# Kernel optimization log

Measured on AMD Instinct MI355X. Metric: run time of the kernel, lower is better.

The kernel has to match this reference:

```python
import jax, jax.numpy as jnp
import numpy as np

BASE_TEMP, MIN_TEMP, MAX_TEMP = 0.07, 0.04, 0.2
B, D = 4096, 768


def setup_inputs() -> dict:
    key = jax.random.key(0)
    k1, k2, k3 = jax.random.split(key, 3)
    return {
        "vision_features": jax.random.normal(k1, (B, D), dtype=jnp.float32),
        "text_features": jax.random.normal(k2, (B, D), dtype=jnp.float32),
        "match_ids": jax.random.randint(k3, (B,), 0, 1024, dtype=jnp.int64),
    }


def reference(vision_features, text_features, match_ids):
    # L2-normalize features along the feature dim
    v = vision_features / jnp.linalg.norm(vision_features, axis=1, keepdims=True)
    t = text_features / jnp.linalg.norm(text_features, axis=1, keepdims=True)
    sim = v @ t.T  # [B, B]

    n = match_ids.shape[0]
    match = match_ids[:, None] == match_ids[None, :]  # [B, B] bool, diag True
    mf = match.astype(sim.dtype)
    eye = jnp.eye(n, dtype=sim.dtype)
    pos_mask = mf * (1.0 - eye)          # diagonal zeroed
    neg_mask = 1.0 - mf                   # diagonal also zero (was match)

    pos_mean = (pos_mask * sim).sum() / jnp.maximum(1.0, pos_mask.sum())
    neg_mean = (neg_mask * sim).sum() / jnp.maximum(1.0, neg_mask.sum())
    separation = pos_mean - neg_mean
    temp = jnp.clip(BASE_TEMP * (0.8 + 0.4 * jnp.exp(-2.0 * separation)),
                    MIN_TEMP, MAX_TEMP)

    logits = sim / temp
    # v2t: for each row i, sum over positives j of (-logits[i,j] + lse(row i))
    lse_rows = jax.nn.logsumexp(logits, axis=1)  # [B]
    v2t = (mf * (lse_rows[:, None] - logits)).sum()
    # t2v: for each column i, sum over positives j of (-logits[j,i] + lse(col i))
    lse_cols = jax.nn.logsumexp(logits, axis=0)  # [B]
    t2v = (mf * (lse_cols[None, :] - logits)).sum()

    num_pos = mf.sum()  # includes diagonal, matching the torch code
    v2t = v2t / num_pos
    t2v = t2v / num_pos
    loss = (v2t + t2v) / 2.0
    return loss
```

## Files before the change

kernel.cpp:

```cpp
#include <hip/hip_runtime.h>
#include <hip/hip_bf16.h>

#define NB 4096
#define DD 768
#define NKT 24
#define NBLK 256

typedef __bf16 bf16x8 __attribute__((ext_vector_type(8)));
typedef float f32x4 __attribute__((ext_vector_type(4)));
typedef unsigned int uint;

#define WAITVM(N) asm volatile("s_waitcnt vmcnt(" #N ")" ::: "memory")

__global__ void init_kernel(float* scal)
{
    if (threadIdx.x < 16) scal[threadIdx.x] = 0.0f;
}

__device__ __forceinline__ void stage_range(
    __hip_bfloat16* ldsAll,
    const __hip_bfloat16* __restrict__ vhat, const __hip_bfloat16* __restrict__ that_,
    int rowBase, int colBase, int T, int i0, int i1, int wid, int lane)
{
    int u = T & 3;
    int k0 = T * 32;
    const __hip_bfloat16* src = (wid >= 4) ? that_ : vhat;
    int tb = (wid >= 4) ? colBase : rowBase;
    int w4 = wid & 3;
    int logc = (lane & 3) ^ ((lane >> 3) & 3);
    int rowIn = w4 * 64 + (lane >> 2);
    __hip_bfloat16* dbase = ldsAll + u * 16384 + ((wid >= 4) ? 8192 : 0) + w4 * 2048;
    #pragma unroll
    for (int i = i0; i <= i1; ++i) {
        const __hip_bfloat16* g = src + (size_t)(tb + rowIn + i * 16) * DD + k0 + logc * 8;
        __builtin_amdgcn_global_load_lds(
            (const __attribute__((address_space(1))) void*)g,
            (__attribute__((address_space(3))) void*)(dbase + i * 512),
            16, 0, 0);
    }
}

__global__ __launch_bounds__(512, 2) void fused_kernel(
    const float* __restrict__ vf, const float* __restrict__ tf, const int* __restrict__ ids,
    __hip_bfloat16* __restrict__ vhat, __hip_bfloat16* __restrict__ that_,
    float* scal, float* rs, float* cs, float* cntf, int* npart, uint* bar,
    float* __restrict__ out)
{
    __shared__ __hip_bfloat16 ldsAll[4 * 16384];
    __shared__ int idr[256], idc[256];
    __shared__ float red[24];
    __shared__ float rs_l[256], cs_l[256];
    __shared__ int bp[16], wred_i[8];
    __shared__ float ra[8], rn[8];
    __shared__ float invT_sh, mf_sh;

    int rawb = blockIdx.x;
    int t = threadIdx.x, wid = t >> 6, lane = t & 63;

    {
        f32x4 xr[4][3];
        __hip_bfloat16* dsts[4];
        #pragma unroll
        for (int it = 0; it < 4; ++it) {
            int row = rawb * 32 + wid * 4 + it;
            const float* src;
            if (row < NB) { src = vf + (size_t)row * DD; dsts[it] = vhat + (size_t)row * DD; }
            else          { src = tf + (size_t)(row - NB) * DD; dsts[it] = that_ + (size_t)(row - NB) * DD; }
            xr[it][0] = __builtin_nontemporal_load((const f32x4*)(src + lane * 4));
            xr[it][1] = __builtin_nontemporal_load((const f32x4*)(src + 256 + lane * 4));
            xr[it][2] = __builtin_nontemporal_load((const f32x4*)(src + 512 + lane * 4));
        }
        int idreg[8];
        #pragma unroll
        for (int i = 0; i < 8; ++i) idreg[i] = ids[t + i * 512];

        #pragma unroll
        for (int it = 0; it < 4; ++it) {
            float s = 0.f;
            #pragma unroll
            for (int c = 0; c < 3; ++c)
                s += xr[it][c][0]*xr[it][c][0] + xr[it][c][1]*xr[it][c][1]
                   + xr[it][c][2]*xr[it][c][2] + xr[it][c][3]*xr[it][c][3];
            #pragma unroll
            for (int off = 1; off < 64; off <<= 1) s += __shfl_xor(s, off, 64);
            float scale = 1.0f / sqrtf(s);
            unsigned short* dsh = (unsigned short*)dsts[it];
            #pragma unroll
            for (int c = 0; c < 3; ++c) {
                ushort4 o;
                o.x = __builtin_bit_cast(unsigned short, __float2bfloat16(xr[it][c][0] * scale));
                o.y = __builtin_bit_cast(unsigned short, __float2bfloat16(xr[it][c][1] * scale));
                o.z = __builtin_bit_cast(unsigned short, __float2bfloat16(xr[it][c][2] * scale));
                o.w = __builtin_bit_cast(unsigned short, __float2bfloat16(xr[it][c][3] * scale));
                *(ushort4*)(dsh + c * 256 + lane * 4) = o;
            }
        }
        int* idsh = (int*)ldsAll;
        #pragma unroll
        for (int i = 0; i < 8; ++i) idsh[t + i * 512] = idreg[i];
    }
    __syncthreads();

    {
        int* idsh = (int*)ldsAll;
        int sub = t >> 5, l32 = t & 31;
        int my = idsh[rawb * 16 + sub];
        const int4* idsh4 = (const int4*)idsh;
        int c = 0;
        #pragma unroll 8
        for (int j = l32; j < NB / 4; j += 32) {
            int4 v = idsh4[j];
            c += (v.x == my) + (v.y == my) + (v.z == my) + (v.w == my);
        }
        #pragma unroll
        for (int off = 16; off > 0; off >>= 1) c += __shfl_down(c, off, 32);
        if (l32 == 0) { cntf[rawb * 16 + sub] = (float)c; bp[sub] = c; }
    }
    if (t < 32) rs[rawb * 32 + t] = 0.0f;
    __syncthreads();
    if (t == 0) {
        int s = 0;
        #pragma unroll
        for (int i = 0; i < 16; ++i) s += bp[i];
        npart[rawb] = s;
    }

    __syncthreads();
    if (t == 0) {
        __hip_atomic_fetch_add(bar, 1u, __ATOMIC_ACQ_REL, __HIP_MEMORY_SCOPE_AGENT);
        while (__hip_atomic_load(bar, __ATOMIC_ACQUIRE, __HIP_MEMORY_SCOPE_AGENT) < NBLK)
            __builtin_amdgcn_s_sleep(2);
    }
    __syncthreads();

    int rg = rawb & 7, sq = rawb >> 3;
    int by = (rg >> 1) * 4 + (sq >> 3);
    int bx = (rg & 1) * 8 + (sq & 7);
    int rowBase = by * 256, colBase = bx * 256;
    int wr = wid >> 2, wc = wid & 3;
    int fr = lane & 15, g = lane >> 4;

    f32x4 acc[8][4];
    #pragma unroll
    for (int m = 0; m < 8; ++m)
        #pragma unroll
        for (int n = 0; n < 4; ++n) acc[m][n] = (f32x4){0.f, 0.f, 0.f, 0.f};

    int pcoff = ((g ^ ((fr >> 1) & 3)) * 8);
    int aoff = (wr * 128 + fr) * 32 + pcoff;
    int boff = 8192 + (wc * 64 + fr) * 32 + pcoff;

    stage_range(ldsAll, vhat, that_, rowBase, colBase, 0, 0, 3, wid, lane);
    stage_range(ldsAll, vhat, that_, rowBase, colBase, 1, 0, 3, wid, lane);
    stage_range(ldsAll, vhat, that_, rowBase, colBase, 2, 0, 3, wid, lane);
    WAITVM(8);
    __builtin_amdgcn_s_barrier();

    for (int T = 0; T < NKT; ++T) {
        const __hip_bfloat16* U = ldsAll + (T & 3) * 16384;
        bf16x8 a0[4], bb[4];
        #pragma unroll
        for (int m = 0; m < 4; ++m) a0[m] = *(const bf16x8*)(U + aoff + m * 512);
        #pragma unroll
        for (int n = 0; n < 4; ++n) bb[n] = *(const bf16x8*)(U + boff + n * 512);
        if (T + 3 < NKT)
            stage_range(ldsAll, vhat, that_, rowBase, colBase, T + 3, 0, 1, wid, lane);
        __builtin_amdgcn_s_barrier();
        __builtin_amdgcn_s_setprio(1);
        #pragma unroll
        for (int m = 0; m < 4; ++m)
            #pragma unroll
            for (int n = 0; n < 4; ++n)
                acc[m][n] = __builtin_amdgcn_mfma_f32_16x16x32_bf16(a0[m], bb[n], acc[m][n], 0, 0, 0);
        __builtin_amdgcn_s_setprio(0);
        __builtin_amdgcn_s_barrier();
        bf16x8 a1[4];
        #pragma unroll
        for (int m = 0; m < 4; ++m) a1[m] = *(const bf16x8*)(U + aoff + (m + 4) * 512);
        if (T + 3 < NKT)
            stage_range(ldsAll, vhat, that_, rowBase, colBase, T + 3, 2, 3, wid, lane);
        __builtin_amdgcn_s_barrier();
        __builtin_amdgcn_s_setprio(1);
        #pragma unroll
        for (int m = 0; m < 4; ++m)
            #pragma unroll
            for (int n = 0; n < 4; ++n)
                acc[m + 4][n] = __builtin_amdgcn_mfma_f32_16x16x32_bf16(a1[m], bb[n], acc[m + 4][n], 0, 0, 0);
        __builtin_amdgcn_s_setprio(0);
        if (T < NKT - 3)       { WAITVM(8); }
        else if (T == NKT - 3) { WAITVM(4); }
        else if (T == NKT - 2) { WAITVM(0); }
        __builtin_amdgcn_s_barrier();
    }

    if (t < 256) idr[t] = ids[rowBase + t];
    else         idc[t - 256] = ids[colBase + (t - 256)];
    __syncthreads();
    {
        float tsum = 0.f, msum = 0.f, dsum = 0.f;
        #pragma unroll
        for (int m = 0; m < 8; ++m) {
            int rl = wr * 128 + m * 16 + g * 4;
            #pragma unroll
            for (int n = 0; n < 4; ++n) {
                int cl = wc * 64 + n * 16 + fr;
                int colId = idc[cl];
                int gj = colBase + cl;
                #pragma unroll
                for (int r = 0; r < 4; ++r) {
                    float val = acc[m][n][r];
                    tsum += val;
                    if (idr[rl + r] == colId) msum += val;
                    if (rowBase + rl + r == gj) dsum += val;
                }
            }
        }
        #pragma unroll
        for (int off = 32; off > 0; off >>= 1) {
            tsum += __shfl_down(tsum, off, 64);
            msum += __shfl_down(msum, off, 64);
            dsum += __shfl_down(dsum, off, 64);
        }
        if (lane == 0) { red[wid] = tsum; red[8 + wid] = msum; red[16 + wid] = dsum; }
        __syncthreads();
        if (t == 0) {
            float s0 = 0.f, s1 = 0.f, s2 = 0.f;
            #pragma unroll
            for (int w = 0; w < 8; ++w) { s0 += red[w]; s1 += red[8 + w]; s2 += red[16 + w]; }
            atomicAdd(&scal[0], s0);
            atomicAdd(&scal[1], s1);
            atomicAdd(&scal[2], s2);
        }
    }

    __syncthreads();
    if (t == 0) {
        __hip_atomic_fetch_add(bar, 1u, __ATOMIC_ACQ_REL, __HIP_MEMORY_SCOPE_AGENT);
        while (__hip_atomic_load(bar, __ATOMIC_ACQUIRE, __HIP_MEMORY_SCOPE_AGENT) < 2 * NBLK)
            __builtin_amdgcn_s_sleep(2);
    }
    __syncthreads();

    {
        int myn = (t < NBLK) ? npart[t] : 0;
        #pragma unroll
        for (int off = 32; off > 0; off >>= 1) myn += __shfl_down(myn, off, 64);
        if (lane == 0) wred_i[wid] = myn;
        __syncthreads();
        if (t == 0) {
            int npi = 0;
            #pragma unroll
            for (int w = 0; w < 8; ++w) npi += wred_i[w];
            float total = __hip_atomic_load(&scal[0], __ATOMIC_RELAXED, __HIP_MEMORY_SCOPE_AGENT);
            float mf    = __hip_atomic_load(&scal[1], __ATOMIC_RELAXED, __HIP_MEMORY_SCOPE_AGENT);
            float trace = __hip_atomic_load(&scal[2], __ATOMIC_RELAXED, __HIP_MEMORY_SCOPE_AGENT);
            float np = (float)npi;
            float pos_cnt = np - (float)NB;
            float neg_cnt = (float)NB * (float)NB - np;
            float pos_mean = (mf - trace) / fmaxf(1.0f, pos_cnt);
            float neg_mean = (total - mf) / fmaxf(1.0f, neg_cnt);
            float sep = pos_mean - neg_mean;
            float temp = 0.07f * (0.8f + 0.4f * expf(-2.0f * sep));
            temp = fminf(fmaxf(temp, 0.04f), 0.2f);
            invT_sh = 1.0f / temp;
            mf_sh = mf;
        }
        if (t < 256) { rs_l[t] = 0.0f; cs_l[t] = 0.0f; }
        __syncthreads();
    }
    float invT = invT_sh;

    #pragma unroll
    for (int m = 0; m < 8; ++m)
        #pragma unroll
        for (int n = 0; n < 4; ++n)
            #pragma unroll
            for (int r = 0; r < 4; ++r)
                acc[m][n][r] = __expf((acc[m][n][r] - 1.0f) * invT);
    #pragma unroll
    for (int m = 0; m < 8; ++m) {
        #pragma unroll
        for (int r = 0; r < 4; ++r) {
            float rp = 0.f;
            #pragma unroll
            for (int n = 0; n < 4; ++n) rp += acc[m][n][r];
            rp += __shfl_xor(rp, 1, 64);
            rp += __shfl_xor(rp, 2, 64);
            rp += __shfl_xor(rp, 4, 64);
            rp += __shfl_xor(rp, 8, 64);
            if (fr == 0) atomicAdd(&rs_l[wr * 128 + m * 16 + g * 4 + r], rp);
        }
    }
    #pragma unroll
    for (int n = 0; n < 4; ++n) {
        float cp = 0.f;
        #pragma unroll
        for (int m = 0; m < 8; ++m)
            #pragma unroll
            for (int r = 0; r < 4; ++r) cp += acc[m][n][r];
        cp += __shfl_xor(cp, 16, 64);
        cp += __shfl_xor(cp, 32, 64);
        if (g == 0) atomicAdd(&cs_l[wc * 64 + n * 16 + fr], cp);
    }
    __syncthreads();
    if (t < 256) {
        atomicAdd(&rs[rowBase + t], rs_l[t]);
        atomicAdd(&cs[colBase + t], cs_l[t]);
    }

    __syncthreads();
    if (t == 0)
        __hip_atomic_fetch_add(bar, 1u, __ATOMIC_ACQ_REL, __HIP_MEMORY_SCOPE_AGENT);
    if (rawb != 0) return;
    if (t == 0) {
        while (__hip_atomic_load(bar, __ATOMIC_ACQUIRE, __HIP_MEMORY_SCOPE_AGENT) < 3 * NBLK)
            __builtin_amdgcn_s_sleep(2);
    }
    __syncthreads();

    {
        float a = 0.f, npl = 0.f;
        for (int i = t; i < NB; i += 512) {
            float cf = cntf[i];
            a += cf * (logf(rs[i]) + logf(cs[i]));
            npl += cf;
        }
        #pragma unroll
        for (int off = 32; off > 0; off >>= 1) {
            a += __shfl_down(a, off, 64);
            npl += __shfl_down(npl, off, 64);
        }
        if (lane == 0) { ra[wid] = a; rn[wid] = npl; }
        __syncthreads();
        if (t == 0) {
            float A = 0.f, np = 0.f;
            #pragma unroll
            for (int w = 0; w < 8; ++w) { A += ra[w]; np += rn[w]; }
            out[0] = (A + 2.0f * invT_sh * (np - mf_sh)) / (2.0f * np);
        }
    }
}

extern "C" void kernel_launch(void* const* d_in, const int* in_sizes, int n_in,
                              void* d_out, int out_size, void* d_ws, size_t ws_size,
                              hipStream_t stream)
{
    const float* vf  = (const float*)d_in[0];
    const float* tf  = (const float*)d_in[1];
    const int*   ids = (const int*)d_in[2];

    float* ws_f = (float*)d_ws;
    float* scal = ws_f;
    float* rs   = ws_f + 16;
    float* cs   = ws_f + 16 + 4096;
    float* cntf = ws_f + 16 + 8192;
    int* npart  = (int*)(ws_f + 16 + 12288);
    uint* bar   = (uint*)(scal + 6);
    __hip_bfloat16* vhat  = (__hip_bfloat16*)((char*)d_ws + 131072);
    __hip_bfloat16* that_ = vhat + (size_t)NB * DD;

    init_kernel<<<1, 64, 0, stream>>>(scal);
    fused_kernel<<<NBLK, 512, 0, stream>>>(vf, tf, ids, vhat, that_,
                                           scal, rs, cs, cntf, npart, bar, (float*)d_out);
}
```

Before: 91.05 us.

## Quantize normalized features to FP8 and run similarity GEMM with FP8 MFMA

The normalization pass now writes the L2-normalized features as packed FP8 (e4m3) instead of bf16, in a permuted dword layout. The GEMM stages 64-byte K chunks into LDS and issues pairs of 16x16x32 FP8 MFMAs per fragment, which halves the number of K iterations. The aim is to halve global and LDS traffic and cut the loop's barrier count. The MFMA count stays the same, and the lower-precision similarities, later divided by a small temperature, may hurt the accuracy of the loss.

```diff
diff --git a/kernel.cpp b/kernel.cpp
--- a/kernel.cpp
+++ b/kernel.cpp
@@ -3,11 +3,11 @@
 
 #define NB 4096
 #define DD 768
-#define NKT 24
+#define NKT 12
 #define NBLK 256
 
-typedef __bf16 bf16x8 __attribute__((ext_vector_type(8)));
 typedef float f32x4 __attribute__((ext_vector_type(4)));
+typedef long i64x2 __attribute__((ext_vector_type(2)));
 typedef unsigned int uint;
 
 #define WAITVM(N) asm volatile("s_waitcnt vmcnt(" #N ")" ::: "memory")
@@ -18,35 +18,34 @@
 }
 
 __device__ __forceinline__ void stage_range(
-    __hip_bfloat16* ldsAll,
-    const __hip_bfloat16* __restrict__ vhat, const __hip_bfloat16* __restrict__ that_,
+    unsigned char* ldsAll,
+    const unsigned char* __restrict__ vhat8, const unsigned char* __restrict__ that8,
     int rowBase, int colBase, int T, int i0, int i1, int wid, int lane)
 {
     int u = T & 3;
-    int k0 = T * 32;
-    const __hip_bfloat16* src = (wid >= 4) ? that_ : vhat;
+    const unsigned char* src = (wid >= 4) ? that8 : vhat8;
     int tb = (wid >= 4) ? colBase : rowBase;
     int w4 = wid & 3;
     int logc = (lane & 3) ^ ((lane >> 3) & 3);
     int rowIn = w4 * 64 + (lane >> 2);
-    __hip_bfloat16* dbase = ldsAll + u * 16384 + ((wid >= 4) ? 8192 : 0) + w4 * 2048;
+    unsigned char* dbase = ldsAll + u * 32768 + ((wid >= 4) ? 16384 : 0) + w4 * 4096;
     #pragma unroll
     for (int i = i0; i <= i1; ++i) {
-        const __hip_bfloat16* g = src + (size_t)(tb + rowIn + i * 16) * DD + k0 + logc * 8;
+        const unsigned char* g = src + (size_t)(tb + rowIn + i * 16) * DD + T * 64 + logc * 16;
         __builtin_amdgcn_global_load_lds(
             (const __attribute__((address_space(1))) void*)g,
-            (__attribute__((address_space(3))) void*)(dbase + i * 512),
+            (__attribute__((address_space(3))) void*)(dbase + i * 1024),
             16, 0, 0);
     }
 }
 
 __global__ __launch_bounds__(512, 2) void fused_kernel(
     const float* __restrict__ vf, const float* __restrict__ tf, const int* __restrict__ ids,
-    __hip_bfloat16* __restrict__ vhat, __hip_bfloat16* __restrict__ that_,
+    unsigned char* __restrict__ vhat8, unsigned char* __restrict__ that8,
     float* scal, float* rs, float* cs, float* cntf, int* npart, uint* bar,
     float* __restrict__ out)
 {
-    __shared__ __hip_bfloat16 ldsAll[4 * 16384];
+    __shared__ unsigned char ldsAll[4 * 32768];
     __shared__ int idr[256], idc[256];
     __shared__ float red[24];
     __shared__ float rs_l[256], cs_l[256];
@@ -59,13 +58,13 @@
 
     {
         f32x4 xr[4][3];
-        __hip_bfloat16* dsts[4];
+        uint* dsts[4];
         #pragma unroll
         for (int it = 0; it < 4; ++it) {
             int row = rawb * 32 + wid * 4 + it;
             const float* src;
-            if (row < NB) { src = vf + (size_t)row * DD; dsts[it] = vhat + (size_t)row * DD; }
-            else          { src = tf + (size_t)(row - NB) * DD; dsts[it] = that_ + (size_t)(row - NB) * DD; }
+            if (row < NB) { src = vf + (size_t)row * DD; dsts[it] = (uint*)(vhat8 + (size_t)row * DD); }
+            else          { src = tf + (size_t)(row - NB) * DD; dsts[it] = (uint*)(that8 + (size_t)(row - NB) * DD); }
             xr[it][0] = __builtin_nontemporal_load((const f32x4*)(src + lane * 4));
             xr[it][1] = __builtin_nontemporal_load((const f32x4*)(src + 256 + lane * 4));
             xr[it][2] = __builtin_nontemporal_load((const f32x4*)(src + 512 + lane * 4));
@@ -84,15 +83,14 @@
             #pragma unroll
             for (int off = 1; off < 64; off <<= 1) s += __shfl_xor(s, off, 64);
             float scale = 1.0f / sqrtf(s);
-            unsigned short* dsh = (unsigned short*)dsts[it];
             #pragma unroll
             for (int c = 0; c < 3; ++c) {
-                ushort4 o;
-                o.x = __builtin_bit_cast(unsigned short, __float2bfloat16(xr[it][c][0] * scale));
-                o.y = __builtin_bit_cast(unsigned short, __float2bfloat16(xr[it][c][1] * scale));
-                o.z = __builtin_bit_cast(unsigned short, __float2bfloat16(xr[it][c][2] * scale));
-                o.w = __builtin_bit_cast(unsigned short, __float2bfloat16(xr[it][c][3] * scale));
-                *(ushort4*)(dsh + c * 256 + lane * 4) = o;
+                int k0 = c * 256 + lane * 4;
+                int dw = (k0 >> 6) * 16 + (((k0 >> 3) & 3) << 2)
+                       + (((k0 >> 5) & 1) << 1) + ((k0 & 7) >> 2);
+                int p = __builtin_amdgcn_cvt_pk_fp8_f32(xr[it][c][0] * scale, xr[it][c][1] * scale, 0, false);
+                p = __builtin_amdgcn_cvt_pk_fp8_f32(xr[it][c][2] * scale, xr[it][c][3] * scale, p, true);
+                dsts[it][dw] = (uint)p;
             }
         }
         int* idsh = (int*)ldsAll;
@@ -146,46 +144,50 @@
         #pragma unroll
         for (int n = 0; n < 4; ++n) acc[m][n] = (f32x4){0.f, 0.f, 0.f, 0.f};
 
-    int pcoff = ((g ^ ((fr >> 1) & 3)) * 8);
-    int aoff = (wr * 128 + fr) * 32 + pcoff;
-    int boff = 8192 + (wc * 64 + fr) * 32 + pcoff;
-
-    stage_range(ldsAll, vhat, that_, rowBase, colBase, 0, 0, 3, wid, lane);
-    stage_range(ldsAll, vhat, that_, rowBase, colBase, 1, 0, 3, wid, lane);
-    stage_range(ldsAll, vhat, that_, rowBase, colBase, 2, 0, 3, wid, lane);
+    int pcoff = (g ^ ((fr >> 1) & 3)) * 16;
+    int aoffB = (wr * 128 + fr) * 64 + pcoff;
+    int boffB = 16384 + (wc * 64 + fr) * 64 + pcoff;
+
+    stage_range(ldsAll, vhat8, that8, rowBase, colBase, 0, 0, 3, wid, lane);
+    stage_range(ldsAll, vhat8, that8, rowBase, colBase, 1, 0, 3, wid, lane);
+    stage_range(ldsAll, vhat8, that8, rowBase, colBase, 2, 0, 3, wid, lane);
     WAITVM(8);
     __builtin_amdgcn_s_barrier();
 
     for (int T = 0; T < NKT; ++T) {
-        const __hip_bfloat16* U = ldsAll + (T & 3) * 16384;
-        bf16x8 a0[4], bb[4];
-        #pragma unroll
-        for (int m = 0; m < 4; ++m) a0[m] = *(const bf16x8*)(U + aoff + m * 512);
-        #pragma unroll
-        for (int n = 0; n < 4; ++n) bb[n] = *(const bf16x8*)(U + boff + n * 512);
+        const unsigned char* U = ldsAll + (T & 3) * 32768;
+        i64x2 a0[4], bb[4];
+        #pragma unroll
+        for (int m = 0; m < 4; ++m) a0[m] = *(const i64x2*)(U + aoffB + m * 1024);
+        #pragma unroll
+        for (int n = 0; n < 4; ++n) bb[n] = *(const i64x2*)(U + boffB + n * 1024);
         if (T + 3 < NKT)
-            stage_range(ldsAll, vhat, that_, rowBase, colBase, T + 3, 0, 1, wid, lane);
+            stage_range(ldsAll, vhat8, that8, rowBase, colBase, T + 3, 0, 1, wid, lane);
         __builtin_amdgcn_s_barrier();
         __builtin_amdgcn_s_setprio(1);
         #pragma unroll
         for (int m = 0; m < 4; ++m)
             #pragma unroll
-            for (int n = 0; n < 4; ++n)
-                acc[m][n] = __builtin_amdgcn_mfma_f32_16x16x32_bf16(a0[m], bb[n], acc[m][n], 0, 0, 0);
+            for (int n = 0; n < 4; ++n) {
+                acc[m][n] = __builtin_amdgcn_mfma_f32_16x16x32_fp8_fp8(a0[m][0], bb[n][0], acc[m][n], 0, 0, 0);
+                acc[m][n] = __builtin_amdgcn_mfma_f32_16x16x32_fp8_fp8(a0[m][1], bb[n][1], acc[m][n], 0, 0, 0);
+            }
         __builtin_amdgcn_s_setprio(0);
         __builtin_amdgcn_s_barrier();
-        bf16x8 a1[4];
-        #pragma unroll
-        for (int m = 0; m < 4; ++m) a1[m] = *(const bf16x8*)(U + aoff + (m + 4) * 512);
+        i64x2 a1[4];
+        #pragma unroll
+        for (int m = 0; m < 4; ++m) a1[m] = *(const i64x2*)(U + aoffB + (m + 4) * 1024);
         if (T + 3 < NKT)
-            stage_range(ldsAll, vhat, that_, rowBase, colBase, T + 3, 2, 3, wid, lane);
+            stage_range(ldsAll, vhat8, that8, rowBase, colBase, T + 3, 2, 3, wid, lane);
         __builtin_amdgcn_s_barrier();
         __builtin_amdgcn_s_setprio(1);
         #pragma unroll
         for (int m = 0; m < 4; ++m)
             #pragma unroll
-            for (int n = 0; n < 4; ++n)
-                acc[m + 4][n] = __builtin_amdgcn_mfma_f32_16x16x32_bf16(a1[m], bb[n], acc[m + 4][n], 0, 0, 0);
+            for (int n = 0; n < 4; ++n) {
+                acc[m + 4][n] = __builtin_amdgcn_mfma_f32_16x16x32_fp8_fp8(a1[m][0], bb[n][0], acc[m + 4][n], 0, 0, 0);
+                acc[m + 4][n] = __builtin_amdgcn_mfma_f32_16x16x32_fp8_fp8(a1[m][1], bb[n][1], acc[m + 4][n], 0, 0, 0);
+            }
         __builtin_amdgcn_s_setprio(0);
         if (T < NKT - 3)       { WAITVM(8); }
         else if (T == NKT - 3) { WAITVM(4); }
@@ -356,10 +358,10 @@
     float* cntf = ws_f + 16 + 8192;
     int* npart  = (int*)(ws_f + 16 + 12288);
     uint* bar   = (uint*)(scal + 6);
-    __hip_bfloat16* vhat  = (__hip_bfloat16*)((char*)d_ws + 131072);
-    __hip_bfloat16* that_ = vhat + (size_t)NB * DD;
+    unsigned char* vhat8 = (unsigned char*)d_ws + 131072;
+    unsigned char* that8 = vhat8 + (size_t)NB * DD;
 
     init_kernel<<<1, 64, 0, stream>>>(scal);
-    fused_kernel<<<NBLK, 512, 0, stream>>>(vf, tf, ids, vhat, that_,
+    fused_kernel<<<NBLK, 512, 0, stream>>>(vf, tf, ids, vhat8, that8,
                                            scal, rs, cs, cntf, npart, bar, (float*)d_out);
 }
```

Measured after the change: 85.09 us. 1.07x faster.
